# Kernel optimization log

Hardware: AMD Instinct MI355X
Metric: run time of the kernel (lower is better)

The kernel has to match this reference:

```python
import jax, jax.numpy as jnp
import numpy as np

B, S, D, H, C = 128, 2048, 128, 128, 10  # batch, seq_len, input_size, hidden_size, num_classes


def setup_inputs() -> dict:
    key = jax.random.key(0)
    ks = jax.random.split(key, 11)
    k = 1.0 / np.sqrt(H)  # PyTorch RNN init scale
    u = lambda kk, shp: jax.random.uniform(kk, shp, jnp.float32, -k, k)
    return {
        "x": jax.random.normal(ks[0], (B, S, D), jnp.float32),
        # layer 0 (input D -> hidden H); gate order: r, z, n (PyTorch convention)
        "W_ih0": u(ks[1], (3 * H, D)), "W_hh0": u(ks[2], (3 * H, H)),
        "b_ih0": u(ks[3], (3 * H,)),   "b_hh0": u(ks[4], (3 * H,)),
        # layer 1 (hidden H -> hidden H)
        "W_ih1": u(ks[5], (3 * H, H)), "W_hh1": u(ks[6], (3 * H, H)),
        "b_ih1": u(ks[7], (3 * H,)),   "b_hh1": u(ks[8], (3 * H,)),
        # output linear H -> C
        "W_out": u(ks[9], (C, H)), "b_out": u(ks[10], (C,)),
    }


def _gru_layer(x, W_ih, W_hh, b_ih, b_hh):
    """Single unidirectional GRU layer, PyTorch math. x: [B,S,Din] -> ([B,S,H], h_last [B,H])."""
    Bs = x.shape[0]
    Hh = W_hh.shape[1]
    # Precompute all input projections in one big GEMM: [S,B,3H]
    xp = jnp.einsum('bsd,gd->sbg', x, W_ih) + b_ih
    h0 = jnp.zeros((Bs, Hh), x.dtype)

    def step(h, xp_t):
        hp = h @ W_hh.T + b_hh                      # [B,3H]
        xr, xz, xn = jnp.split(xp_t, 3, axis=-1)
        hr, hz, hn = jnp.split(hp, 3, axis=-1)
        r = jax.nn.sigmoid(xr + hr)                 # reset gate
        z = jax.nn.sigmoid(xz + hz)                 # update gate
        n = jnp.tanh(xn + r * hn)                   # new gate
        h_new = (1.0 - z) * n + z * h
        return h_new, h_new

    h_last, hs = jax.lax.scan(step, h0, xp)         # hs: [S,B,H]
    return jnp.transpose(hs, (1, 0, 2)), h_last


def reference(x, W_ih0, W_hh0, b_ih0, b_hh0, W_ih1, W_hh1, b_ih1, b_hh1, W_out, b_out):
    y0, _ = _gru_layer(x, W_ih0, W_hh0, b_ih0, b_hh0)
    _, h_last = _gru_layer(y0, W_ih1, W_hh1, b_ih1, b_hh1)
    # dropout between layers is disabled at inference (eval mode)
    return h_last @ W_out.T + b_out                 # [B,C] logits
```

## Files before the change

kernel.cpp:

```cpp
#include <hip/hip_runtime.h>
#include <hip/hip_bf16.h>


using bf16x8 = __attribute__((ext_vector_type(8))) short;
using s16x4  = __attribute__((ext_vector_type(4))) short;
using f32x4  = __attribute__((ext_vector_type(4))) float;
using f16x8  = __attribute__((ext_vector_type(8))) _Float16;
using f16x4  = __attribute__((ext_vector_type(4))) _Float16;
using u32x2  = __attribute__((ext_vector_type(2))) unsigned int;

#define S_LEN 2048
#define D_IN  128
#define HID   128
#define B_TOT 128
#define BC    16
#define PAD   136
#define G3    384
#define M_TOT (B_TOT * S_LEN)

#define CH    32
#define WIN   4
#define TILE_HALFS (BC * HID)
#define WGWIN_HALFS (WIN * CH * TILE_HALFS)

__device__ __forceinline__ float bf2f(short s) {
  unsigned int u = ((unsigned int)(unsigned short)s) << 16;
  float f; __builtin_memcpy(&f, &u, 4); return f;
}
__device__ __forceinline__ short f2bf(float f) {
  unsigned int u; __builtin_memcpy(&u, &f, 4);
  u += 0x7fffu + ((u >> 16) & 1u);
  return (short)(u >> 16);
}
__device__ __forceinline__ float fast_sigmoid(float x) {
  return __builtin_amdgcn_rcpf(1.f + __expf(-x));
}
__device__ __forceinline__ float fast_tanh(float x) {
  return 2.f * __builtin_amdgcn_rcpf(1.f + __expf(-2.f * x)) - 1.f;
}
__device__ __forceinline__ f32x4 MFMA(bf16x8 a, bf16x8 b, f32x4 c) {
  return __builtin_amdgcn_mfma_f32_16x16x32_bf16(a, b, c, 0, 0, 0);
}
__device__ __forceinline__ f32x4 MFMA16(f16x8 a, f16x8 b, f32x4 c) {
  return __builtin_amdgcn_mfma_f32_16x16x32_f16(a, b, c, 0, 0, 0);
}
__device__ __forceinline__ void loadA(bf16x8 (&a)[4], const short* p) {
#pragma unroll
  for (int kq = 0; kq < 4; ++kq) a[kq] = *(const bf16x8*)(p + kq * 32);
}
__device__ __forceinline__ void loadA16(f16x8 (&a)[4], const _Float16* p) {
#pragma unroll
  for (int kq = 0; kq < 4; ++kq) a[kq] = *(const f16x8*)(p + kq * 32);
}
__device__ __forceinline__ void wg_barrier() {
  asm volatile("s_waitcnt lgkmcnt(0)\n\ts_barrier" ::: "memory");
}
__device__ __forceinline__ int ld_acq(const int* p) {
  return __hip_atomic_load(p, __ATOMIC_ACQUIRE, __HIP_MEMORY_SCOPE_AGENT);
}
__device__ __forceinline__ int ld_rlx(const int* p) {
  return __hip_atomic_load(p, __ATOMIC_RELAXED, __HIP_MEMORY_SCOPE_AGENT);
}
__device__ __forceinline__ void st_rel(int* p, int v) {
  __hip_atomic_store(p, v, __ATOMIC_RELEASE, __HIP_MEMORY_SCOPE_AGENT);
}

__global__ __launch_bounds__(256, 1) void xp0_gemm(
    const float* __restrict__ x, const float* __restrict__ Wih0,
    const float* __restrict__ bih0, const float* __restrict__ bhh0,
    _Float16* __restrict__ xp0)
{
  __shared__ _Float16 wlds[96 * PAD];
  __shared__ float bfold[G3];

  const int tid = threadIdx.x;
  const int w = tid >> 6, lane = tid & 63, nw = lane & 15, quad = lane >> 4;
  const int m0 = blockIdx.x * 64 + w * 16;

  for (int g = tid; g < G3; g += 256)
    bfold[g] = bih0[g] + (g < 256 ? bhh0[g] : 0.f);

  f16x8 af[4];
  const int arow = m0 + nw;
#pragma unroll
  for (int kq = 0; kq < 4; ++kq) {
    const float* p = x + (size_t)arow * D_IN + kq * 32 + quad * 8;
    float4 v0 = *(const float4*)p, v1 = *(const float4*)(p + 4);
    af[kq] = (f16x8){(_Float16)v0.x, (_Float16)v0.y, (_Float16)v0.z, (_Float16)v0.w,
                     (_Float16)v1.x, (_Float16)v1.y, (_Float16)v1.z, (_Float16)v1.w};
  }

  for (int grp = 0; grp < 4; ++grp) {
    __syncthreads();
    for (int i = tid; i < 96 * 128 / 4; i += 256) {
      const int idx = i * 4, row = idx >> 7, cc = idx & 127;
      float4 v = *(const float4*)(Wih0 + (size_t)(grp * 96 + row) * 128 + cc);
      f16x4 s = { (_Float16)v.x, (_Float16)v.y, (_Float16)v.z, (_Float16)v.w };
      *(f16x4*)&wlds[row * PAD + cc] = s;
    }
    __syncthreads();

    f32x4 acc[6];
#pragma unroll
    for (int i = 0; i < 6; ++i) acc[i] = (f32x4){0.f, 0.f, 0.f, 0.f};
#pragma unroll
    for (int tI = 0; tI < 6; ++tI)
#pragma unroll
      for (int kq = 0; kq < 4; ++kq) {
        f16x8 b = *(const f16x8*)&wlds[(tI * 16 + nw) * PAD + kq * 32 + quad * 8];
        acc[tI] = MFMA16(af[kq], b, acc[tI]);
      }

#pragma unroll
    for (int tI = 0; tI < 6; ++tI) {
      const int g = grp * 96 + tI * 16 + nw;
      const float bb = bfold[g];
#pragma unroll
      for (int rr = 0; rr < 4; ++rr) {
        const int m = m0 + quad * 4 + rr;
        xp0[(size_t)m * G3 + g] = (_Float16)(acc[tI][rr] + bb);
      }
    }
  }
}

__device__ __forceinline__ void mm3f(const f16x8 (&a)[4], const f16x8 (&W)[3][4],
                                     f32x4& r, f32x4& z, f32x4& n) {
#pragma unroll
  for (int kq = 0; kq < 4; ++kq) {
    r = MFMA16(a[kq], W[0][kq], r);
    z = MFMA16(a[kq], W[1][kq], z);
    n = MFMA16(a[kq], W[2][kq], n);
  }
}
__device__ __forceinline__ void mm3x2f(const f16x8 (&a)[4],
    const f16x8 (&Wa)[3][4], const f16x8 (&Wb)[3][4],
    f32x4& r1, f32x4& z1, f32x4& n1, f32x4& r2, f32x4& z2, f32x4& n2) {
#pragma unroll
  for (int kq = 0; kq < 4; ++kq) {
    r1 = MFMA16(a[kq], Wa[0][kq], r1);
    r2 = MFMA16(a[kq], Wb[0][kq], r2);
    z1 = MFMA16(a[kq], Wa[1][kq], z1);
    z2 = MFMA16(a[kq], Wb[1][kq], z2);
    n1 = MFMA16(a[kq], Wa[2][kq], n1);
    n2 = MFMA16(a[kq], Wb[2][kq], n2);
  }
}

__global__ __launch_bounds__(512, 2) void gru2_split(
    const _Float16* __restrict__ xp0,
    _Float16* __restrict__ win,
    int* __restrict__ ctrl,
    const float* __restrict__ Whh0, const float* __restrict__ bhh0,
    const float* __restrict__ Wih1, const float* __restrict__ Whh1,
    const float* __restrict__ bih1, const float* __restrict__ bhh1,
    const float* __restrict__ Wout, const float* __restrict__ bout,
    float* __restrict__ out)
{
  __shared__ _Float16 hf[2][BC * PAD];

  const int bid  = blockIdx.x;
  const int role = bid >> 3;
  const int g    = bid & 7;
  const int tid  = threadIdx.x;
  const int w    = tid >> 6;
  const int lane = tid & 63;
  const int nw   = lane & 15;
  const int quad = lane >> 4;
  const int col  = w * 16 + nw;
  const int b0   = g * BC;
  const int aoff = nw * PAD + quad * 8;

  int* flagp = ctrl + g;
  int* consp = ctrl + 8 + g;
  _Float16* win_g = win + (size_t)g * WGWIN_HALFS;

  for (int i = tid; i < 2 * BC * PAD; i += 512)
    ((_Float16*)hf)[i] = (_Float16)0.f;

  if (role == 0) {
    const float b0n_h = bhh0[256 + col];
    f16x8 Wh0[3][4];
#pragma unroll
    for (int gg = 0; gg < 3; ++gg)
#pragma unroll
      for (int kq = 0; kq < 4; ++kq) {
        const size_t o = (size_t)(gg * 128 + col) * HID + kq * 32 + quad * 8;
#pragma unroll
        for (int e = 0; e < 8; ++e) Wh0[gg][kq][e] = (_Float16)Whh0[o + e];
      }

    size_t xbase[4];
#pragma unroll
    for (int rr = 0; rr < 4; ++rr)
      xbase[rr] = (size_t)(b0 + quad * 4 + rr) * S_LEN * G3 + col;

    float PA[12], PB[12];
#pragma unroll
    for (int gg = 0; gg < 3; ++gg)
#pragma unroll
      for (int rr = 0; rr < 4; ++rr)
        PA[gg * 4 + rr] = (float)xp0[xbase[rr] + gg * 128];

    f32x4 h0r = {0.f, 0.f, 0.f, 0.f};
    const int cpo = (tid >> 5) * PAD + ((4 * tid) & 127);
    int cons_seen = 0;
    __syncthreads();

    auto pstep = [&](float (&P)[12], float (&Pn)[12], const int t,
                     const int pr, const int pw) {
      if ((t & (CH - 1)) == 0) {
        const int need = (t >> 5) - (WIN - 1);
        if (need > 0 && cons_seen < need) {
          do { cons_seen = ld_rlx(consp);
               if (cons_seen < need) __builtin_amdgcn_s_sleep(8);
          } while (cons_seen < need);
        }
      }
      const int tn = (t + 1 < S_LEN) ? t + 1 : t;
#pragma unroll
      for (int gg = 0; gg < 3; ++gg)
#pragma unroll
        for (int rr = 0; rr < 4; ++rr)
          Pn[gg * 4 + rr] = (float)xp0[xbase[rr] + (size_t)tn * G3 + gg * 128];

      f32x4 ar = {P[0], P[1], P[2], P[3]};
      f32x4 az = {P[4], P[5], P[6], P[7]};
      f32x4 ahn = {b0n_h, b0n_h, b0n_h, b0n_h};
      f16x8 a[4];
      loadA16(a, &hf[pr][aoff]);
      mm3f(a, Wh0, ar, az, ahn);
#pragma unroll
      for (int rr = 0; rr < 4; ++rr) {
        float r = fast_sigmoid(ar[rr]);
        float z = fast_sigmoid(az[rr]);
        float n = fast_tanh(P[8 + rr] + r * ahn[rr]);
        float h = n + z * (h0r[rr] - n);
        h0r[rr] = h;
        hf[pw][(quad * 4 + rr) * PAD + col] = (_Float16)h;
      }
      wg_barrier();
      {
        u32x2 v;
        __builtin_memcpy(&v, &hf[pw][cpo], 8);
        _Float16* dst = win_g +
            ((size_t)((t >> 5) & (WIN - 1)) * CH + (t & (CH - 1))) * TILE_HALFS
            + 4 * tid;
        __builtin_nontemporal_store(v, (u32x2*)dst);
      }
      if ((t & (CH - 1)) == (CH - 1)) {
        __syncthreads();
        if (tid == 0) st_rel(flagp, (t >> 5) + 1);
      }
    };

#pragma unroll 1
    for (int tt = 0; tt < S_LEN; tt += 2) {
      pstep(PA, PB, tt,     0, 1);
      pstep(PB, PA, tt + 1, 1, 0);
    }
  } else {
    const float b1r   = bih1[col]       + bhh1[col];
    const float b1z   = bih1[128 + col] + bhh1[128 + col];
    const float b1n_i = bih1[256 + col];
    const float b1n_h = bhh1[256 + col];

    f16x8 Wi1[3][4], Wh1[3][4];
#pragma unroll
    for (int gg = 0; gg < 3; ++gg)
#pragma unroll
      for (int kq = 0; kq < 4; ++kq) {
        const size_t o = (size_t)(gg * 128 + col) * HID + kq * 32 + quad * 8;
#pragma unroll
        for (int e = 0; e < 8; ++e) {
          Wi1[gg][kq][e] = (_Float16)Wih1[o + e];
          Wh1[gg][kq][e] = (_Float16)Whh1[o + e];
        }
      }

    const int afroff = nw * 128 + quad * 8;
    f32x4 h1r = {0.f, 0.f, 0.f, 0.f};
    int seen = 0;
    __syncthreads();

    while (seen < 1) { seen = ld_acq(flagp);
                       if (seen < 1) __builtin_amdgcn_s_sleep(8); }
    f16x8 Anext[4];
    f32x4 xp1r = {b1r, b1r, b1r, b1r};
    f32x4 xp1z = {b1z, b1z, b1z, b1z};
    f32x4 xp1n = {b1n_i, b1n_i, b1n_i, b1n_i};
    {
      f16x8 A0[4];
#pragma unroll
      for (int kq = 0; kq < 4; ++kq)
        A0[kq] = *(const f16x8*)(win_g + afroff + kq * 32);
      mm3f(A0, Wi1, xp1r, xp1z, xp1n);
    }
#pragma unroll
    for (int kq = 0; kq < 4; ++kq)
      Anext[kq] = *(const f16x8*)(win_g + TILE_HALFS + afroff + kq * 32);

    auto cstep = [&](const int t, const int pr, const int pw) {
      if ((t & (CH - 1)) == 0 && tid == 0) st_rel(consp, t >> 5);
      f16x8 hfr[4];
      loadA16(hfr, &hf[pr][aoff]);
      f32x4 br  = xp1r;
      f32x4 bz  = xp1z;
      f32x4 bxn = xp1n;
      f32x4 bhn = {b1n_h, b1n_h, b1n_h, b1n_h};
      mm3f(hfr, Wh1, br, bz, bhn);
#pragma unroll
      for (int rr = 0; rr < 4; ++rr) {
        float r = fast_sigmoid(br[rr]);
        float z = fast_sigmoid(bz[rr]);
        float n = fast_tanh(bxn[rr] + r * bhn[rr]);
        float h = n + z * (h1r[rr] - n);
        h1r[rr] = h;
        hf[pw][(quad * 4 + rr) * PAD + col] = (_Float16)h;
      }
      xp1r = (f32x4){b1r, b1r, b1r, b1r};
      xp1z = (f32x4){b1z, b1z, b1z, b1z};
      xp1n = (f32x4){b1n_i, b1n_i, b1n_i, b1n_i};
      mm3f(Anext, Wi1, xp1r, xp1z, xp1n);
      const int tp2 = (t + 2 < S_LEN) ? t + 2 : S_LEN - 1;
      const int cn2 = (tp2 >> 5) + 1;
      if (seen < cn2) {
        do { seen = ld_acq(flagp);
             if (seen < cn2) __builtin_amdgcn_s_sleep(8);
        } while (seen < cn2);
      }
      {
        const _Float16* tp = win_g +
            ((size_t)((tp2 >> 5) & (WIN - 1)) * CH + (tp2 & (CH - 1))) * TILE_HALFS
            + afroff;
#pragma unroll
        for (int kq = 0; kq < 4; ++kq) Anext[kq] = *(const f16x8*)(tp + kq * 32);
      }
      wg_barrier();
    };

#pragma unroll 1
    for (int tt = 0; tt < S_LEN; tt += 2) {
      cstep(tt,     0, 1);
      cstep(tt + 1, 1, 0);
    }

    if (tid < BC * 10) {
      const int b = tid / 10, c = tid % 10;
      float s = bout[c];
      const _Float16* hh = &hf[0][b * PAD];
#pragma unroll 8
      for (int k = 0; k < HID; ++k)
        s += (float)hh[k] * Wout[c * HID + k];
      out[(size_t)(b0 + b) * 10 + c] = s;
    }
  }
}

__global__ __launch_bounds__(512, 2) void gru2_rec(
    const _Float16* __restrict__ xp0,
    const float* __restrict__ Whh0, const float* __restrict__ bhh0,
    const float* __restrict__ Wih1, const float* __restrict__ Whh1,
    const float* __restrict__ bih1, const float* __restrict__ bhh1,
    const float* __restrict__ Wout, const float* __restrict__ bout,
    float* __restrict__ out)
{
  __shared__ _Float16 h0f[2][BC * PAD];
  __shared__ _Float16 h1f[2][BC * PAD];

  const int tid  = threadIdx.x;
  const int w    = tid >> 6;
  const int lane = tid & 63;
  const int nw   = lane & 15;
  const int quad = lane >> 4;
  const int col  = w * 16 + nw;
  const int b0   = blockIdx.x * BC;

  for (int i = tid; i < 2 * BC * PAD; i += 512) {
    ((_Float16*)h0f)[i] = (_Float16)0.f;
    ((_Float16*)h1f)[i] = (_Float16)0.f;
  }

  const float b0n_h = bhh0[256 + col];
  const float b1r   = bih1[col]       + bhh1[col];
  const float b1z   = bih1[128 + col] + bhh1[128 + col];
  const float b1n_i = bih1[256 + col];
  const float b1n_h = bhh1[256 + col];

  f16x8 Wh0[3][4], Wi1[3][4], Wh1[3][4];
#pragma unroll
  for (int g = 0; g < 3; ++g) {
#pragma unroll
    for (int kq = 0; kq < 4; ++kq) {
      const size_t o = (size_t)(g * 128 + col) * HID + kq * 32 + quad * 8;
#pragma unroll
      for (int e = 0; e < 8; ++e) {
        Wh0[g][kq][e] = (_Float16)Whh0[o + e];
        Wi1[g][kq][e] = (_Float16)Wih1[o + e];
        Wh1[g][kq][e] = (_Float16)Whh1[o + e];
      }
    }
  }

  size_t xbase[4];
#pragma unroll
  for (int rr = 0; rr < 4; ++rr)
    xbase[rr] = (size_t)(b0 + quad * 4 + rr) * S_LEN * G3 + col;

  float P[12];
#pragma unroll
  for (int g = 0; g < 3; ++g)
#pragma unroll
    for (int rr = 0; rr < 4; ++rr)
      P[g * 4 + rr] = (float)xp0[xbase[rr] + g * 128];

  f32x4 h0r = {0.f, 0.f, 0.f, 0.f}, h1r = {0.f, 0.f, 0.f, 0.f};
  wg_barrier();

  const int aoff = nw * PAD + quad * 8;

  for (int t = 0; t < S_LEN; ++t) {
    const int pr = t & 1, pw = pr ^ 1;
    const int tn = (t + 1 < S_LEN) ? t + 1 : t;
    float Pn[12];
#pragma unroll
    for (int g = 0; g < 3; ++g)
#pragma unroll
      for (int rr = 0; rr < 4; ++rr)
        Pn[g * 4 + rr] = (float)xp0[xbase[rr] + (size_t)tn * G3 + g * 128];

    f32x4 ar  = {P[0], P[1], P[2], P[3]};
    f32x4 az  = {P[4], P[5], P[6], P[7]};
    f32x4 ahn = {b0n_h, b0n_h, b0n_h, b0n_h};
    f32x4 br  = {b1r, b1r, b1r, b1r};
    f32x4 bz  = {b1z, b1z, b1z, b1z};
    f32x4 bxn = {b1n_i, b1n_i, b1n_i, b1n_i};
    f32x4 bhn = {b1n_h, b1n_h, b1n_h, b1n_h};

    f16x8 a[4];
    loadA16(a, &h0f[pr][aoff]); mm3x2f(a, Wh0, Wi1, ar, az, ahn, br, bz, bxn);
    loadA16(a, &h1f[pr][aoff]); mm3f(a, Wh1, br, bz, bhn);

#pragma unroll
    for (int rr = 0; rr < 4; ++rr) {
      float r = fast_sigmoid(ar[rr]);
      float z = fast_sigmoid(az[rr]);
      float n = fast_tanh(P[8 + rr] + r * ahn[rr]);
      float h = n + z * (h0r[rr] - n);
      h0r[rr] = h;
      h0f[pw][(quad * 4 + rr) * PAD + col] = (_Float16)h;
    }
    if (t) {
#pragma unroll
      for (int rr = 0; rr < 4; ++rr) {
        float r = fast_sigmoid(br[rr]);
        float z = fast_sigmoid(bz[rr]);
        float n = fast_tanh(bxn[rr] + r * bhn[rr]);
        float h = n + z * (h1r[rr] - n);
        h1r[rr] = h;
        h1f[pw][(quad * 4 + rr) * PAD + col] = (_Float16)h;
      }
    }
#pragma unroll
    for (int i = 0; i < 12; ++i) P[i] = Pn[i];
    wg_barrier();
  }

  {
    f32x4 br  = {b1r, b1r, b1r, b1r};
    f32x4 bz  = {b1z, b1z, b1z, b1z};
    f32x4 bxn = {b1n_i, b1n_i, b1n_i, b1n_i};
    f32x4 bhn = {b1n_h, b1n_h, b1n_h, b1n_h};
    f16x8 a[4];
    loadA16(a, &h0f[0][aoff]); mm3f(a, Wi1, br, bz, bxn);
    loadA16(a, &h1f[0][aoff]); mm3f(a, Wh1, br, bz, bhn);
#pragma unroll
    for (int rr = 0; rr < 4; ++rr) {
      float r = fast_sigmoid(br[rr]);
      float z = fast_sigmoid(bz[rr]);
      float n = fast_tanh(bxn[rr] + r * bhn[rr]);
      float h = n + z * (h1r[rr] - n);
      h1f[1][(quad * 4 + rr) * PAD + col] = (_Float16)h;
    }
    wg_barrier();
  }

  if (tid < BC * 10) {
    const int b = tid / 10, c = tid % 10;
    float s = bout[c];
    const _Float16* hh = &h1f[1][b * PAD];
#pragma unroll 8
    for (int k = 0; k < HID; ++k)
      s += (float)hh[k] * Wout[c * HID + k];
    out[(size_t)(b0 + b) * 10 + c] = s;
  }
}

template<bool NSEP>
__device__ __forceinline__ void mm6(const bf16x8 (&a)[4], const bf16x8 (&W)[6][4],
                                    f32x4 (&acc)[6], f32x4 (&accn)[2]) {
#pragma unroll
  for (int tI = 0; tI < 6; ++tI)
#pragma unroll
    for (int kq = 0; kq < 4; ++kq) {
      if (NSEP && tI >= 4) accn[tI - 4] = MFMA(a[kq], W[tI][kq], accn[tI - 4]);
      else                 acc[tI]      = MFMA(a[kq], W[tI][kq], acc[tI]);
    }
}

__global__ __launch_bounds__(256, 1) void gru2_v1(
    const float* __restrict__ x,
    const float* __restrict__ Wih0, const float* __restrict__ Whh0,
    const float* __restrict__ bih0, const float* __restrict__ bhh0,
    const float* __restrict__ Wih1, const float* __restrict__ Whh1,
    const float* __restrict__ bih1, const float* __restrict__ bhh1,
    const float* __restrict__ Wout, const float* __restrict__ bout,
    float* __restrict__ out)
{
  __shared__ short h0hi[2][BC * PAD], h0lo[2][BC * PAD];
  __shared__ short h1hi[2][BC * PAD], h1lo[2][BC * PAD];
  __shared__ short xbhi[2][BC * PAD], xblo[2][BC * PAD];

  const int tid = threadIdx.x, w = tid >> 6, lane = tid & 63;
  const int nw = lane & 15, quad = lane >> 4, u0 = w * 32;
  const int b0 = blockIdx.x * BC;

  for (int i = tid; i < BC * PAD; i += 256) {
    h0hi[0][i] = 0; h0lo[0][i] = 0; h1hi[0][i] = 0; h1lo[0][i] = 0;
  }
  const size_t xelem = (size_t)(b0 + (tid >> 4)) * (size_t)(S_LEN * D_IN) + (size_t)((tid & 15) * 8);
  const int xsoff = (tid >> 4) * PAD + (tid & 15) * 8;

  auto load_x = [&](int t, bf16x8& xhi, bf16x8& xlo) {
    const size_t o = xelem + (size_t)t * D_IN;
    float4 v0 = *(const float4*)(x + o), v1 = *(const float4*)(x + o + 4);
    float v[8] = {v0.x, v0.y, v0.z, v0.w, v1.x, v1.y, v1.z, v1.w};
#pragma unroll
    for (int e = 0; e < 8; ++e) {
      short h = f2bf(v[e]); xhi[e] = h; xlo[e] = f2bf(v[e] - bf2f(h));
    }
  };
  { bf16x8 xh, xl; load_x(0, xh, xl);
    *(bf16x8*)&xbhi[0][xsoff] = xh; *(bf16x8*)&xblo[0][xsoff] = xl; }

  float brz0[4], bn0[4], brz1[4], bn1[4];
#pragma unroll
  for (int i = 0; i < 2; ++i) {
    const int c = u0 + i * 16 + nw;
    brz0[i] = bih0[c] + bhh0[c];     brz0[2 + i] = bih0[128 + c] + bhh0[128 + c];
    bn0[i] = bih0[256 + c];          bn0[2 + i] = bhh0[256 + c];
    brz1[i] = bih1[c] + bhh1[c];     brz1[2 + i] = bih1[128 + c] + bhh1[128 + c];
    bn1[i] = bih1[256 + c];          bn1[2 + i] = bhh1[256 + c];
  }

  bf16x8 W0[6][4], Wh0f[6][4], W1[6][4], Wh1f[6][4];
#pragma unroll
  for (int tI = 0; tI < 6; ++tI) {
    const int rb = (tI >> 1) * 128 + u0 + (tI & 1) * 16 + nw;
#pragma unroll
    for (int kq = 0; kq < 4; ++kq) {
      const size_t o = (size_t)rb * HID + kq * 32 + quad * 8;
#pragma unroll
      for (int e = 0; e < 8; ++e) {
        W0[tI][kq][e] = f2bf(Wih0[o + e]);  Wh0f[tI][kq][e] = f2bf(Whh0[o + e]);
        W1[tI][kq][e] = f2bf(Wih1[o + e]);  Wh1f[tI][kq][e] = f2bf(Whh1[o + e]);
      }
    }
  }

  f32x4 h0reg[2] = {{0,0,0,0},{0,0,0,0}}, h1reg[2] = {{0,0,0,0},{0,0,0,0}};
  const f32x4 ZV = {0.f, 0.f, 0.f, 0.f};
  __syncthreads();
  const int aoff = nw * PAD + quad * 8;

  auto gates = [&](const f32x4 (&acc)[6], const f32x4 (&accn)[2], f32x4 (&hreg)[2],
                   const float (&brz)[4], const float (&bn)[4],
                   short* dhi, short* dlo) {
#pragma unroll
    for (int i = 0; i < 2; ++i) {
      const int c = u0 + i * 16 + nw;
#pragma unroll
      for (int rr = 0; rr < 4; ++rr) {
        float rv = fast_sigmoid(acc[i][rr] + brz[i]);
        float zv = fast_sigmoid(acc[2 + i][rr] + brz[2 + i]);
        float nv = fast_tanh((acc[4 + i][rr] + bn[i]) + rv * (accn[i][rr] + bn[2 + i]));
        float h = (1.f - zv) * nv + zv * hreg[i][rr];
        hreg[i][rr] = h;
        short hi = f2bf(h);
        const int row = quad * 4 + rr;
        dhi[row * PAD + c] = hi;
        dlo[row * PAD + c] = f2bf(h - bf2f(hi));
      }
    }
  };

  for (int t = 0; t < S_LEN; ++t) {
    const int pr = t & 1, pw = pr ^ 1;
    const int t1 = (t + 1 < S_LEN) ? t + 1 : t;
    bf16x8 xh, xl; load_x(t1, xh, xl);

    f32x4 acc[6], accn[2];
#pragma unroll
    for (int i = 0; i < 6; ++i) acc[i] = ZV;
#pragma unroll
    for (int i = 0; i < 2; ++i) accn[i] = ZV;
    bf16x8 a[4];
    loadA(a, &xbhi[pr][aoff]); mm6<false>(a, W0, acc, accn);
    loadA(a, &xblo[pr][aoff]); mm6<false>(a, W0, acc, accn);
    loadA(a, &h0hi[pr][aoff]); mm6<true >(a, Wh0f, acc, accn);
    loadA(a, &h0lo[pr][aoff]); mm6<true >(a, Wh0f, acc, accn);
    gates(acc, accn, h0reg, brz0, bn0, h0hi[pw], h0lo[pw]);
    __syncthreads();

#pragma unroll
    for (int i = 0; i < 6; ++i) acc[i] = ZV;
#pragma unroll
    for (int i = 0; i < 2; ++i) accn[i] = ZV;
    loadA(a, &h0hi[pw][aoff]); mm6<false>(a, W1, acc, accn);
    loadA(a, &h0lo[pw][aoff]); mm6<false>(a, W1, acc, accn);
    loadA(a, &h1hi[pr][aoff]); mm6<true >(a, Wh1f, acc, accn);
    loadA(a, &h1lo[pr][aoff]); mm6<true >(a, Wh1f, acc, accn);
    *(bf16x8*)&xbhi[pw][xsoff] = xh;
    *(bf16x8*)&xblo[pw][xsoff] = xl;
    gates(acc, accn, h1reg, brz1, bn1, h1hi[pw], h1lo[pw]);
    __syncthreads();
  }

  if (tid < BC * 10) {
    const int b = tid / 10, c = tid % 10;
    float s = bout[c];
    const short* hh = &h1hi[0][b * PAD];
    const short* hl = &h1lo[0][b * PAD];
#pragma unroll 8
    for (int k = 0; k < HID; ++k)
      s += (bf2f(hh[k]) + bf2f(hl[k])) * Wout[c * HID + k];
    out[(size_t)(b0 + b) * 10 + c] = s;
  }
}

extern "C" void kernel_launch(void* const* d_in, const int* in_sizes, int n_in,
                              void* d_out, int out_size, void* d_ws, size_t ws_size,
                              hipStream_t stream) {
  (void)in_sizes; (void)n_in; (void)out_size;
  const float* x    = (const float*)d_in[0];
  const float* Wih0 = (const float*)d_in[1];
  const float* Whh0 = (const float*)d_in[2];
  const float* bih0 = (const float*)d_in[3];
  const float* bhh0 = (const float*)d_in[4];
  const float* Wih1 = (const float*)d_in[5];
  const float* Whh1 = (const float*)d_in[6];
  const float* bih1 = (const float*)d_in[7];
  const float* bhh1 = (const float*)d_in[8];
  const float* Wout = (const float*)d_in[9];
  const float* bout = (const float*)d_in[10];
  float* out = (float*)d_out;

  const size_t XPB  = (size_t)M_TOT * G3 * sizeof(_Float16);
  const size_t WINB = 8ull * WGWIN_HALFS * sizeof(_Float16);
  const size_t REQ  = XPB + WINB + 64;

  if (ws_size >= REQ) {
    char* ws = (char*)d_ws;
    _Float16* xp0  = (_Float16*)ws;
    _Float16* wing = (_Float16*)(ws + XPB);
    int*      ctrl = (int*)(ws + XPB + WINB);
    (void)hipMemsetAsync(ctrl, 0, 64, stream);
    xp0_gemm<<<dim3(M_TOT / 64), dim3(256), 0, stream>>>(
        x, Wih0, bih0, bhh0, xp0);
    gru2_split<<<dim3(16), dim3(512), 0, stream>>>(
        xp0, wing, ctrl, Whh0, bhh0, Wih1, Whh1, bih1, bhh1, Wout, bout, out);
  } else if (ws_size >= XPB) {
    xp0_gemm<<<dim3(M_TOT / 64), dim3(256), 0, stream>>>(
        x, Wih0, bih0, bhh0, (_Float16*)d_ws);
    gru2_rec<<<dim3(B_TOT / BC), dim3(512), 0, stream>>>(
        (const _Float16*)d_ws, Whh0, bhh0, Wih1, Whh1, bih1, bhh1, Wout, bout, out);
  } else {
    gru2_v1<<<dim3(B_TOT / BC), dim3(256), 0, stream>>>(
        x, Wih0, Whh0, bih0, bhh0, Wih1, Whh1, bih1, bhh1, Wout, bout, out);
  }
}
```

Before: 2.162 ms.

## Make input-projection GEMM persistent with LDS-staged coalesced stores; prefetch xp two steps ahead

The input-projection GEMM becomes a persistent kernel with 256 blocks. Each block loads one gate's 128x128 weight into LDS once and loops over many 64-row tiles of x. Those tiles are staged in LDS, and results go back through LDS so each row writes contiguous 16-byte chunks instead of scattered 2-byte stores. Separately, the layer-0 recurrence now prefetches xp for step t+2 after the current step's work rather than t+1 at the start, giving the loads more latency slack. The trade-offs are reading x three times (once per gate) and adding extra barriers per tile.

New measurement: 2.401 ms. 1.11x slower.

```diff
diff --git a/kernel.cpp b/kernel.cpp
--- a/kernel.cpp
+++ b/kernel.cpp
@@ -23,6 +23,10 @@
 #define TILE_HALFS (BC * HID)
 #define WGWIN_HALFS (WIN * CH * TILE_HALFS)
 
+#define PADW  136
+#define MBLK  64
+#define NBLK  (M_TOT / MBLK / 256)
+
 __device__ __forceinline__ float bf2f(short s) {
   unsigned int u = ((unsigned int)(unsigned short)s) << 16;
   float f; __builtin_memcpy(&f, &u, 4); return f;
@@ -65,60 +69,77 @@
   __hip_atomic_store(p, v, __ATOMIC_RELEASE, __HIP_MEMORY_SCOPE_AGENT);
 }
 
-__global__ __launch_bounds__(256, 1) void xp0_gemm(
+__global__ __launch_bounds__(256, 1) void xp0_gemm2(
     const float* __restrict__ x, const float* __restrict__ Wih0,
     const float* __restrict__ bih0, const float* __restrict__ bhh0,
     _Float16* __restrict__ xp0)
 {
-  __shared__ _Float16 wlds[96 * PAD];
+  __shared__ _Float16 wlds[128 * PADW];
+  __shared__ _Float16 ald[MBLK * PADW];
   __shared__ float bfold[G3];
 
   const int tid = threadIdx.x;
-  const int w = tid >> 6, lane = tid & 63, nw = lane & 15, quad = lane >> 4;
-  const int m0 = blockIdx.x * 64 + w * 16;
+  const int wv = tid >> 6, lane = tid & 63, nw = lane & 15, quad = lane >> 4;
 
   for (int g = tid; g < G3; g += 256)
     bfold[g] = bih0[g] + (g < 256 ? bhh0[g] : 0.f);
 
-  f16x8 af[4];
-  const int arow = m0 + nw;
-#pragma unroll
-  for (int kq = 0; kq < 4; ++kq) {
-    const float* p = x + (size_t)arow * D_IN + kq * 32 + quad * 8;
-    float4 v0 = *(const float4*)p, v1 = *(const float4*)(p + 4);
-    af[kq] = (f16x8){(_Float16)v0.x, (_Float16)v0.y, (_Float16)v0.z, (_Float16)v0.w,
-                     (_Float16)v1.x, (_Float16)v1.y, (_Float16)v1.z, (_Float16)v1.w};
-  }
-
-  for (int grp = 0; grp < 4; ++grp) {
+  for (int gate = 0; gate < 3; ++gate) {
     __syncthreads();
-    for (int i = tid; i < 96 * 128 / 4; i += 256) {
+    for (int i = tid; i < 128 * 128 / 4; i += 256) {
       const int idx = i * 4, row = idx >> 7, cc = idx & 127;
-      float4 v = *(const float4*)(Wih0 + (size_t)(grp * 96 + row) * 128 + cc);
-      f16x4 s = { (_Float16)v.x, (_Float16)v.y, (_Float16)v.z, (_Float16)v.w };
-      *(f16x4*)&wlds[row * PAD + cc] = s;
+      float4 v = *(const float4*)(Wih0 + (size_t)(gate * 128 + row) * 128 + cc);
+      f16x4 s = {(_Float16)v.x, (_Float16)v.y, (_Float16)v.z, (_Float16)v.w};
+      *(f16x4*)&wlds[row * PADW + cc] = s;
     }
     __syncthreads();
 
-    f32x4 acc[6];
-#pragma unroll
-    for (int i = 0; i < 6; ++i) acc[i] = (f32x4){0.f, 0.f, 0.f, 0.f};
-#pragma unroll
-    for (int tI = 0; tI < 6; ++tI)
-#pragma unroll
-      for (int kq = 0; kq < 4; ++kq) {
-        f16x8 b = *(const f16x8*)&wlds[(tI * 16 + nw) * PAD + kq * 32 + quad * 8];
-        acc[tI] = MFMA16(af[kq], b, acc[tI]);
-      }
-
-#pragma unroll
-    for (int tI = 0; tI < 6; ++tI) {
-      const int g = grp * 96 + tI * 16 + nw;
-      const float bb = bfold[g];
-#pragma unroll
-      for (int rr = 0; rr < 4; ++rr) {
-        const int m = m0 + quad * 4 + rr;
-        xp0[(size_t)m * G3 + g] = (_Float16)(acc[tI][rr] + bb);
+    float bb[8];
+#pragma unroll
+    for (int tI = 0; tI < 8; ++tI) bb[tI] = bfold[gate * 128 + tI * 16 + nw];
+
+    for (int blk = 0; blk < NBLK; ++blk) {
+      const int m0 = (blockIdx.x * NBLK + blk) * MBLK;
+      __syncthreads();
+      for (int i = tid; i < MBLK * 128 / 4; i += 256) {
+        const int idx = i * 4, row = idx >> 7, cc = idx & 127;
+        float4 v = *(const float4*)(x + (size_t)(m0 + row) * D_IN + cc);
+        f16x4 s = {(_Float16)v.x, (_Float16)v.y, (_Float16)v.z, (_Float16)v.w};
+        *(f16x4*)&ald[row * PADW + cc] = s;
+      }
+      __syncthreads();
+
+      f16x8 af[4];
+#pragma unroll
+      for (int kq = 0; kq < 4; ++kq)
+        af[kq] = *(const f16x8*)&ald[(wv * 16 + nw) * PADW + kq * 32 + quad * 8];
+
+      f32x4 acc[8];
+#pragma unroll
+      for (int i = 0; i < 8; ++i) acc[i] = (f32x4){0.f, 0.f, 0.f, 0.f};
+#pragma unroll
+      for (int tI = 0; tI < 8; ++tI)
+#pragma unroll
+        for (int kq = 0; kq < 4; ++kq) {
+          f16x8 b = *(const f16x8*)&wlds[(tI * 16 + nw) * PADW + kq * 32 + quad * 8];
+          acc[tI] = MFMA16(af[kq], b, acc[tI]);
+        }
+
+#pragma unroll
+      for (int tI = 0; tI < 8; ++tI)
+#pragma unroll
+        for (int rr = 0; rr < 4; ++rr)
+          ald[(wv * 16 + quad * 4 + rr) * PADW + tI * 16 + nw] =
+              (_Float16)(acc[tI][rr] + bb[tI]);
+      __syncthreads();
+
+      {
+        const int row = tid >> 2, cp = (tid & 3) * 32;
+        const _Float16* src = &ald[row * PADW + cp];
+        _Float16* dst = xp0 + (size_t)(m0 + row) * G3 + gate * 128 + cp;
+#pragma unroll
+        for (int j = 0; j < 4; ++j)
+          *(f16x8*)(dst + j * 8) = *(const f16x8*)(src + j * 8);
       }
     }
   }
@@ -195,20 +216,25 @@
     for (int rr = 0; rr < 4; ++rr)
       xbase[rr] = (size_t)(b0 + quad * 4 + rr) * S_LEN * G3 + col;
 
+    auto loadPK = [&](float (&P)[12], int t) {
+      const size_t tG = (size_t)t * G3;
+#pragma unroll
+      for (int gg = 0; gg < 3; ++gg)
+#pragma unroll
+        for (int rr = 0; rr < 4; ++rr)
+          P[gg * 4 + rr] = (float)xp0[xbase[rr] + tG + gg * 128];
+    };
+
     float PA[12], PB[12];
-#pragma unroll
-    for (int gg = 0; gg < 3; ++gg)
-#pragma unroll
-      for (int rr = 0; rr < 4; ++rr)
-        PA[gg * 4 + rr] = (float)xp0[xbase[rr] + gg * 128];
+    loadPK(PA, 0);
+    loadPK(PB, 1);
 
     f32x4 h0r = {0.f, 0.f, 0.f, 0.f};
     const int cpo = (tid >> 5) * PAD + ((4 * tid) & 127);
     int cons_seen = 0;
     __syncthreads();
 
-    auto pstep = [&](float (&P)[12], float (&Pn)[12], const int t,
-                     const int pr, const int pw) {
+    auto pstep = [&](float (&P)[12], const int t, const int pr, const int pw) {
       if ((t & (CH - 1)) == 0) {
         const int need = (t >> 5) - (WIN - 1);
         if (need > 0 && cons_seen < need) {
@@ -217,12 +243,6 @@
           } while (cons_seen < need);
         }
       }
-      const int tn = (t + 1 < S_LEN) ? t + 1 : t;
-#pragma unroll
-      for (int gg = 0; gg < 3; ++gg)
-#pragma unroll
-        for (int rr = 0; rr < 4; ++rr)
-          Pn[gg * 4 + rr] = (float)xp0[xbase[rr] + (size_t)tn * G3 + gg * 128];
 
       f32x4 ar = {P[0], P[1], P[2], P[3]};
       f32x4 az = {P[4], P[5], P[6], P[7]};
@@ -252,12 +272,14 @@
         __syncthreads();
         if (tid == 0) st_rel(flagp, (t >> 5) + 1);
       }
+      const int tn = (t + 2 < S_LEN) ? t + 2 : t;
+      loadPK(P, tn);
     };
 
 #pragma unroll 1
     for (int tt = 0; tt < S_LEN; tt += 2) {
-      pstep(PA, PB, tt,     0, 1);
-      pstep(PB, PA, tt + 1, 1, 0);
+      pstep(PA, tt,     0, 1);
+      pstep(PB, tt + 1, 1, 0);
     }
   } else {
     const float b1r   = bih1[col]       + bhh1[col];
@@ -665,12 +687,12 @@
     _Float16* wing = (_Float16*)(ws + XPB);
     int*      ctrl = (int*)(ws + XPB + WINB);
     (void)hipMemsetAsync(ctrl, 0, 64, stream);
-    xp0_gemm<<<dim3(M_TOT / 64), dim3(256), 0, stream>>>(
+    xp0_gemm2<<<dim3(256), dim3(256), 0, stream>>>(
         x, Wih0, bih0, bhh0, xp0);
     gru2_split<<<dim3(16), dim3(512), 0, stream>>>(
         xp0, wing, ctrl, Whh0, bhh0, Wih1, Whh1, bih1, bhh1, Wout, bout, out);
   } else if (ws_size >= XPB) {
-    xp0_gemm<<<dim3(M_TOT / 64), dim3(256), 0, stream>>>(
+    xp0_gemm2<<<dim3(256), dim3(256), 0, stream>>>(
         x, Wih0, bih0, bhh0, (_Float16*)d_ws);
     gru2_rec<<<dim3(B_TOT / BC), dim3(512), 0, stream>>>(
         (const _Float16*)d_ws, Whh0, bhh0, Wih1, Whh1, bih1, bhh1, Wout, bout, out);
```
